# Performance work log

Measured on AMD Instinct MI355X. Metric: run time of the kernel, lower is better.

## Reference

```python
import jax, jax.numpy as jnp
import numpy as np

OFFSETS = list(range(0, 8))  # s_prev=0, s_curr=7 -> kernel_size K=8
NEG = -1e9  # finite stand-in for -inf in masked softmax (avoids NaN rows)


def setup_inputs() -> dict:
    key = jax.random.key(0)
    ks = jax.random.split(key, 5)
    B, N, d = 8, 4096, 256
    x = jax.random.normal(ks[0], (B, N, d), dtype=jnp.float32)
    # most-recent-first: index 0 has smallest time delta -> sorted ascending
    delta_times = jnp.sort(jax.random.uniform(ks[1], (B, N), dtype=jnp.float32) * 100.0, axis=1)
    lengths = jax.random.randint(ks[2], (B,), N // 2, N + 1)
    valid_mask = jnp.arange(N)[None, :] < lengths[:, None]  # [B, N] bool
    w = jax.random.normal(ks[3], (len(OFFSETS),), dtype=jnp.float32) * 0.1
    beta = jax.random.normal(ks[4], (1,), dtype=jnp.float32) * 0.1
    return {"x": x, "delta_times": delta_times, "valid_mask": valid_mask, "w": w, "beta": beta}


def _mixer(x, delta_times, valid_mask, w, beta):
    B, N, d = x.shape
    sxs, tds, cvs = [], [], []
    for p in OFFSETS:  # small fixed kernel window, K=8
        if p == 0:
            sxs.append(x)
            tds.append(jnp.zeros((B, N), x.dtype))
            cvs.append(valid_mask)
        else:
            sxs.append(jnp.pad(x[:, p:], ((0, 0), (0, p), (0, 0))))
            tds.append(jnp.pad(jnp.maximum(delta_times[:, p:] - delta_times[:, :N - p], 0.0), ((0, 0), (0, p))))
            cvs.append(jnp.pad(valid_mask[:, p:] & valid_mask[:, :N - p], ((0, 0), (0, p))))
    sx = jnp.stack(sxs, axis=2)  # [B, N, K, d]
    td = jnp.stack(tds, axis=2)  # [B, N, K]
    cv = jnp.stack(cvs, axis=2)  # [B, N, K] bool
    # temporal-decay softmax over offsets (masked positions -> ~0 weight)
    theta = jax.nn.softmax(jnp.where(cv, -td, NEG), axis=2)
    wsm = jax.nn.softmax(w)[None, None, :]  # learnable per-offset weights
    b = jax.nn.sigmoid(beta[0])
    alpha = jnp.where(cv, b * wsm + (1.0 - b) * theta, 0.0)
    alpha = alpha / jnp.maximum(alpha.sum(axis=2, keepdims=True), 1e-8)
    out = jnp.einsum('bnkd,bnk->bnd', sx, alpha)
    return out * valid_mask[..., None].astype(x.dtype)


def reference(x, delta_times, valid_mask, w, beta):
    # Dropout is identity in eval mode.
    return _mixer(x, delta_times, valid_mask, w, beta)
```

## Files before the change

kernel.cpp:

```cpp
#include <hip/hip_runtime.h>


#define NEGV (-1e9f)

constexpr int Bc = 8;
constexpr int Nc = 4096;
constexpr int D4 = 64;
constexpr int Rw = 8;
constexpr int XR = 15;

__global__ __launch_bounds__(256) void atm_kernel(
    const float* __restrict__ x,
    const float* __restrict__ dt,
    const void* __restrict__ maskp,
    const float* __restrict__ w,
    const float* __restrict__ beta,
    float* __restrict__ out)
{
    const int tid = threadIdx.x;
    const int lane = tid & 63;
    const int gw = blockIdx.x * 4 + (tid >> 6);
    const int waves_per_b = Nc / Rw;
    const int b = gw / waves_per_b;
    const int n0 = (gw % waves_per_b) * Rw;
    const long row0 = (long)b * Nc + n0;

    const int r_l = lane >> 3;
    const int p_l = lane & 7;
    const int n = n0 + r_l;
    const long rowm = row0 + r_l;

    const unsigned char* m8 = (const unsigned char*)maskp;
    const int* m32 = (const int*)maskp;
    const bool is_byte = (m8[1] != 0);
    auto getm = [&](long i) -> bool {
        return is_byte ? (m8[i] != 0) : (m32[i] != 0);
    };

    bool c;
    float td = 0.f;
    if (p_l == 0) {
        c = getm(rowm);
    } else if (n + p_l < Nc) {
        c = getm(rowm) && getm(rowm + p_l);
        td = fmaxf(dt[rowm + p_l] - dt[rowm], 0.f);
    } else {
        c = false;
    }
    const float lg = c ? -td : NEGV;

    float mx = lg;
    mx = fmaxf(mx, __shfl_xor(mx, 1));
    mx = fmaxf(mx, __shfl_xor(mx, 2));
    mx = fmaxf(mx, __shfl_xor(mx, 4));
    const float th = expf(lg - mx);
    float tsum = th;
    tsum += __shfl_xor(tsum, 1);
    tsum += __shfl_xor(tsum, 2);
    tsum += __shfl_xor(tsum, 4);

    const float wv = w[p_l];
    float wmax = wv;
    wmax = fmaxf(wmax, __shfl_xor(wmax, 1));
    wmax = fmaxf(wmax, __shfl_xor(wmax, 2));
    wmax = fmaxf(wmax, __shfl_xor(wmax, 4));
    const float we = expf(wv - wmax);
    float wsum = we;
    wsum += __shfl_xor(wsum, 1);
    wsum += __shfl_xor(wsum, 2);
    wsum += __shfl_xor(wsum, 4);

    const float bsig = 1.0f / (1.0f + expf(-beta[0]));
    const float a = c ? (bsig * we / wsum + (1.0f - bsig) * th / tsum) : 0.f;
    float asum = a;
    asum += __shfl_xor(asum, 1);
    asum += __shfl_xor(asum, 2);
    asum += __shfl_xor(asum, 4);
    const float aval = a / fmaxf(asum, 1e-8f);

    const float4* __restrict__ x4 = (const float4*)x;
    float4 win[XR];
#pragma unroll
    for (int j = 0; j < XR; ++j) {
        win[j] = (n0 + j < Nc) ? x4[(row0 + j) * D4 + lane]
                               : make_float4(0.f, 0.f, 0.f, 0.f);
    }

    float4* __restrict__ out4 = (float4*)out;
#pragma unroll
    for (int r = 0; r < Rw; ++r) {
        float4 acc = make_float4(0.f, 0.f, 0.f, 0.f);
#pragma unroll
        for (int p = 0; p < 8; ++p) {
            const float av = __shfl(aval, r * 8 + p);
            const float4 xv = win[r + p];
            acc.x = fmaf(av, xv.x, acc.x);
            acc.y = fmaf(av, xv.y, acc.y);
            acc.z = fmaf(av, xv.z, acc.z);
            acc.w = fmaf(av, xv.w, acc.w);
        }
        out4[(row0 + r) * D4 + lane] = acc;
    }
}

extern "C" void kernel_launch(void* const* d_in, const int* in_sizes, int n_in,
                              void* d_out, int out_size, void* d_ws, size_t ws_size,
                              hipStream_t stream) {
    const float* x    = (const float*)d_in[0];
    const float* dt   = (const float*)d_in[1];
    const void*  mask = d_in[2];
    const float* w    = (const float*)d_in[3];
    const float* beta = (const float*)d_in[4];
    float* out = (float*)d_out;

    dim3 grid(Bc * Nc / (Rw * 4));
    dim3 block(256);
    atm_kernel<<<grid, block, 0, stream>>>(x, dt, mask, w, beta, out);
}
```

Measured before the change: 90.14 us.

## Split feature dim across two waves, remap blocks, use readlane broadcast

Each 8-row strip is now handled by two waves, each covering half the feature dimension with float2 loads, which doubles the grid and halves per-thread registers. Blocks are remapped by an 8-way interleave (presumably to spread them across XCDs), launch bounds ask for higher occupancy, and the per-offset weight broadcast uses readlane instead of a shuffle. In exchange, the mask/softmax preamble is computed twice per strip, and the narrower loads may be less efficient per instruction.

```diff
diff --git a/kernel.cpp b/kernel.cpp
--- a/kernel.cpp
+++ b/kernel.cpp
@@ -5,11 +5,11 @@
 
 constexpr int Bc = 8;
 constexpr int Nc = 4096;
-constexpr int D4 = 64;
+constexpr int D2 = 128;
 constexpr int Rw = 8;
 constexpr int XR = 15;
 
-__global__ __launch_bounds__(256) void atm_kernel(
+__global__ __launch_bounds__(256, 8) void atm_kernel(
     const float* __restrict__ x,
     const float* __restrict__ dt,
     const void* __restrict__ maskp,
@@ -19,10 +19,16 @@
 {
     const int tid = threadIdx.x;
     const int lane = tid & 63;
-    const int gw = blockIdx.x * 4 + (tid >> 6);
-    const int waves_per_b = Nc / Rw;
-    const int b = gw / waves_per_b;
-    const int n0 = (gw % waves_per_b) * Rw;
+    const int bid = blockIdx.x;
+
+    const int gb = (bid & 7) * 256 + (bid >> 3);
+
+    const int gwave = gb * 4 + (tid >> 6);
+    const int strip = gwave >> 1;
+    const int half  = gwave & 1;
+    const int strips_per_b = Nc / Rw;
+    const int b  = strip / strips_per_b;
+    const int n0 = (strip % strips_per_b) * Rw;
     const long row0 = (long)b * Nc + n0;
 
     const int r_l = lane >> 3;
@@ -78,28 +84,28 @@
     asum += __shfl_xor(asum, 4);
     const float aval = a / fmaxf(asum, 1e-8f);
 
-    const float4* __restrict__ x4 = (const float4*)x;
-    float4 win[XR];
+    const float2* __restrict__ x2 = (const float2*)x;
+    const int col = half * 64 + lane;
+    float2 win[XR];
 #pragma unroll
     for (int j = 0; j < XR; ++j) {
-        win[j] = (n0 + j < Nc) ? x4[(row0 + j) * D4 + lane]
-                               : make_float4(0.f, 0.f, 0.f, 0.f);
+        win[j] = (n0 + j < Nc) ? x2[(row0 + j) * D2 + col]
+                               : make_float2(0.f, 0.f);
     }
 
-    float4* __restrict__ out4 = (float4*)out;
+    float2* __restrict__ out2 = (float2*)out;
 #pragma unroll
     for (int r = 0; r < Rw; ++r) {
-        float4 acc = make_float4(0.f, 0.f, 0.f, 0.f);
+        float2 acc = make_float2(0.f, 0.f);
 #pragma unroll
         for (int p = 0; p < 8; ++p) {
-            const float av = __shfl(aval, r * 8 + p);
-            const float4 xv = win[r + p];
+            const float av = __uint_as_float(
+                __builtin_amdgcn_readlane(__float_as_uint(aval), r * 8 + p));
+            const float2 xv = win[r + p];
             acc.x = fmaf(av, xv.x, acc.x);
             acc.y = fmaf(av, xv.y, acc.y);
-            acc.z = fmaf(av, xv.z, acc.z);
-            acc.w = fmaf(av, xv.w, acc.w);
         }
-        out4[(row0 + r) * D4 + lane] = acc;
+        out2[(row0 + r) * D2 + col] = acc;
     }
 }
 
@@ -113,7 +119,7 @@
     const float* beta = (const float*)d_in[4];
     float* out = (float*)d_out;
 
-    dim3 grid(Bc * Nc / (Rw * 4));
+    dim3 grid(Bc * Nc / Rw * 2 / 4);
     dim3 block(256);
     atm_kernel<<<grid, block, 0, stream>>>(x, dt, mask, w, beta, out);
 }
```

Result: no change. 91.42 us (+1.4%).
